# Kernel tuning notes

Measured on AMD Instinct MI355X. Metric: run time of the kernel, lower is better.

## Reference

```python
import jax, jax.numpy as jnp
import numpy as np

DELTA_VAR = 0.5
DELTA_DIST = 1.5
ALPHA, BETA, GAMMA = 1.0, 1.0, 0.001
EPS = 1e-8


def _safe_sqrt(x):
    # sqrt with zero (sub)gradient at 0, matching torch.norm's subgradient
    pos = x > 0
    return jnp.sqrt(jnp.where(pos, x, 1.0)) * pos


def setup_inputs() -> dict:
    key = jax.random.key(0)
    k1, k2, k3 = jax.random.split(key, 3)
    B, F, H, W, K = 8, 16, 384, 384, 24
    x = jax.random.normal(k1, (B, F, H, W), dtype=jnp.float32)
    n_clusters = jax.random.randint(k2, (B,), 2, K + 1).astype(jnp.int32)
    # per-pixel instance labels, in-range per sample
    labels = jax.random.randint(k3, (B, H * W), 0, K) % n_clusters[:, None]
    target = jax.nn.one_hot(labels, K, dtype=jnp.float32)  # (B, L, K)
    target = target.transpose(0, 2, 1).reshape(B, K, H, W)
    return {"input": x, "target": target, "n_clusters": n_clusters}


def reference(input, target, n_clusters):
    B, F, H, W = input.shape
    K = target.shape[1]
    x = input.reshape(B, F, H * W)          # (b, f, l)
    t = target.reshape(B, K, H * W)         # (b, c, l)
    nc = n_clusters.astype(x.dtype)         # (b,)
    valid = (jnp.arange(K)[None, :] < n_clusters[:, None]).astype(x.dtype)  # (b, c)

    # ---- cluster means (masked segment mean; padded clusters -> 0) ----
    t_sum = t.sum(-1)                                        # (b, c)
    sums = jnp.einsum('bfl,bcl->bfc', x, t)                  # (b, f, c)
    means = sums / (t_sum[:, None, :] + EPS) * valid[:, None, :]

    # ---- variance term: ||x_l - mu_c||_2 via quadratic expansion ----
    x2 = jnp.sum(x * x, axis=1)                              # (b, l)
    m2 = jnp.sum(means * means, axis=1)                      # (b, c)
    xm = jnp.einsum('bfl,bfc->bcl', x, means)                # (b, c, l)
    d2 = jnp.maximum(x2[:, None, :] - 2.0 * xm + m2[:, :, None], 0.0)
    dist = _safe_sqrt(d2)                                    # (b, c, l)
    var = jnp.maximum(dist - DELTA_VAR, 0.0) ** 2 * t        # (b, c, l)
    c_var = var.sum(-1) / (t_sum + EPS)                      # (b, c)
    var_per = (c_var * valid).sum(-1) / (nc + EPS)
    var_term = jnp.sum(var_per * (nc > 0)) / B

    # ---- distance term: hinge on pairwise mean distances ----
    mm = jnp.einsum('bfc,bfd->bcd', means, means)            # (b, c, c)
    pd2 = jnp.maximum(m2[:, :, None] - 2.0 * mm + m2[:, None, :], 0.0)
    pdist = _safe_sqrt(pd2)                                  # (b, c, c)
    offdiag = 1.0 - jnp.eye(K, dtype=x.dtype)
    pair_mask = valid[:, :, None] * valid[:, None, :] * offdiag
    hinge = jnp.maximum(2.0 * DELTA_DIST - pdist, 0.0) ** 2 * pair_mask
    dist_per = hinge.sum((1, 2)) / (2.0 * nc * (nc - 1.0) + EPS)
    dist_term = jnp.sum(dist_per * (nc > 1)) / B

    # ---- regularization term: mean over valid clusters of ||mu_c|| ----
    norms = _safe_sqrt(m2)                                   # (b, c)
    reg_term = jnp.sum((norms * valid).sum(-1) / nc) / B

    return ALPHA * var_term + BETA * dist_term + GAMMA * reg_term
```

## Files before the change

### kernel.cpp

```cpp
#include <hip/hip_runtime.h>

#define B 8
#define F 16
#define K 24
#define L 147456
#define CHUNK1 1024
#define NCH1 144
#define TOTCH 1152
#define EPSF 1e-8f
#define DELTA_VAR 0.5f
#define DELTA_DIST 1.5f
#define GAMMA 0.001f

typedef float fx4 __attribute__((ext_vector_type(4)));
typedef short bf16x8 __attribute__((ext_vector_type(8)));
typedef float f32x4 __attribute__((ext_vector_type(4)));

#define OFF_CNTP 1769472
#define OFF_VARP 1880064
#define OFF_CNT  1990656
#define OFF_MEAN 1991424
#define OFF_LAB  2003968

__device__ __forceinline__ short to_bf16(float v) {
    unsigned u = __float_as_uint(v);
    return (short)((u + 0x7FFFu + ((u >> 16) & 1u)) >> 16);
}

__global__ __launch_bounds__(256, 2) void k1_sums(
        const float* __restrict__ t, const float* __restrict__ x,
        unsigned char* __restrict__ labels, float* __restrict__ cnt_part,
        float* __restrict__ sum_part) {
    const int gblk = blockIdx.x;
    const int b = gblk / NCH1;
    const int ch = gblk % NCH1;
    const int tid = threadIdx.x;
    const int wave = tid >> 6;
    const int lane = tid & 63;

    __shared__ unsigned char slab[CHUNK1];
    __shared__ float hist[4][32];
    __shared__ float sacc[4][F * K];

    if (lane < 32) hist[wave][lane] = 0.f;

    const int px = ch * CHUNK1 + tid * 4;
    const fx4* t4 = (const fx4*)t;
    fx4 tv[K];
    #pragma unroll
    for (int c = 0; c < K; ++c)
        tv[c] = __builtin_nontemporal_load(&t4[((size_t)(b * K + c) * L + px) >> 2]);

    int lab0 = 0, lab1 = 0, lab2 = 0, lab3 = 0;
    #pragma unroll
    for (int c = 0; c < K; ++c) {
        lab0 += c * (tv[c].x > 0.5f);
        lab1 += c * (tv[c].y > 0.5f);
        lab2 += c * (tv[c].z > 0.5f);
        lab3 += c * (tv[c].w > 0.5f);
    }
    uchar4 lv = make_uchar4((unsigned char)lab0, (unsigned char)lab1,
                            (unsigned char)lab2, (unsigned char)lab3);
    *(uchar4*)&labels[(size_t)b * L + px] = lv;
    *(uchar4*)&slab[tid * 4] = lv;
    atomicAdd(&hist[wave][lab0], 1.f);
    atomicAdd(&hist[wave][lab1], 1.f);
    atomicAdd(&hist[wave][lab2], 1.f);
    atomicAdd(&hist[wave][lab3], 1.f);
    __syncthreads();
    if (tid < K) {
        float v = hist[0][tid] + hist[1][tid] + hist[2][tid] + hist[3][tid];
        cnt_part[tid * TOTCH + gblk] = v;
    }

    const int n = lane & 15;
    const int q = lane >> 4;
    const float* xr = x + (size_t)(b * F + n) * L + ch * CHUNK1 + wave * 256 + q * 8;
    fx4 xv[16];
    #pragma unroll
    for (int it = 0; it < 8; ++it) {
        xv[2 * it]     = *(const fx4*)(xr + it * 32);
        xv[2 * it + 1] = *(const fx4*)(xr + it * 32 + 4);
    }

    const unsigned char* sl = slab + wave * 256 + q * 8;
    f32x4 acc0 = {0.f, 0.f, 0.f, 0.f};
    f32x4 acc1 = {0.f, 0.f, 0.f, 0.f};
    #pragma unroll
    for (int it = 0; it < 8; ++it) {
        unsigned l0 = *(const unsigned*)(sl + it * 32);
        unsigned l1 = *(const unsigned*)(sl + it * 32 + 4);
        fx4 xa = xv[2 * it], xc = xv[2 * it + 1];

        bf16x8 afrag;
        afrag[0] = to_bf16(xa.x); afrag[1] = to_bf16(xa.y);
        afrag[2] = to_bf16(xa.z); afrag[3] = to_bf16(xa.w);
        afrag[4] = to_bf16(xc.x); afrag[5] = to_bf16(xc.y);
        afrag[6] = to_bf16(xc.z); afrag[7] = to_bf16(xc.w);

        bf16x8 bf0, bf1;
        #pragma unroll
        for (int j = 0; j < 8; ++j) {
            int lj = (j < 4) ? ((l0 >> (8 * j)) & 0xFF) : ((l1 >> (8 * (j - 4))) & 0xFF);
            bf0[j] = (lj == n)      ? (short)0x3F80 : (short)0;
            bf1[j] = (lj == n + 16) ? (short)0x3F80 : (short)0;
        }
        acc0 = __builtin_amdgcn_mfma_f32_16x16x32_bf16(afrag, bf0, acc0, 0, 0, 0);
        acc1 = __builtin_amdgcn_mfma_f32_16x16x32_bf16(afrag, bf1, acc1, 0, 0, 0);
    }

    #pragma unroll
    for (int r = 0; r < 4; ++r) {
        int f = q * 4 + r;
        sacc[wave][f * K + n] = acc0[r];
        if (n < 8) sacc[wave][f * K + 16 + n] = acc1[r];
    }
    __syncthreads();
    for (int i = tid; i < F * K; i += 256) {
        float v = sacc[0][i] + sacc[1][i] + sacc[2][i] + sacc[3][i];
        sum_part[(size_t)gblk * (F * K) + i] = v;
    }
}

__global__ __launch_bounds__(256) void k2_means(const float* __restrict__ cnt_part,
                                                const float* __restrict__ sum_part,
                                                const int* __restrict__ ncl,
                                                float* __restrict__ counts,
                                                float* __restrict__ means) {
    const int b = blockIdx.x;
    const int tid = threadIdx.x;
    __shared__ float cl[8][K];
    __shared__ float cs[K];

    if (tid < 192) {
        int c = tid >> 3, grp = tid & 7;
        const float* row = cnt_part + c * TOTCH + b * NCH1 + grp * 18;
        float s = 0.f;
        #pragma unroll
        for (int j = 0; j < 18; ++j) s += row[j];
        cl[grp][c] = s;
    }
    __syncthreads();
    if (tid < K) {
        float s = 0.f;
        #pragma unroll
        for (int g = 0; g < 8; ++g) s += cl[g][tid];
        cs[tid] = s;
        counts[b * K + tid] = s;
    }
    __syncthreads();
    const int ncb = ncl[b];
    for (int r = tid; r < F * K; r += 256) {
        float s = 0.f;
        const float* base = sum_part + (size_t)b * NCH1 * (F * K) + r;
        #pragma unroll 4
        for (int j = 0; j < NCH1; ++j) s += base[(size_t)j * (F * K)];
        int c = r % K;
        float valid = (c < ncb) ? 1.f : 0.f;
        means[b * F * K + r] = s / (cs[c] + EPSF) * valid;
    }
}

__global__ __launch_bounds__(256, 2) void k3_var(
        const float* __restrict__ x, const unsigned char* __restrict__ labels,
        const float* __restrict__ means, float* __restrict__ var_part) {
    const int gblk = blockIdx.x;
    const int b = gblk / NCH1;
    const int ch = gblk % NCH1;
    const int tid = threadIdx.x;
    const int wave = tid >> 6;
    const int lane = tid & 63;

    __shared__ float m[F * K];
    __shared__ float hist[4][32];

    const int px = ch * CHUNK1 + tid * 4;
    uchar4 lv = *(const uchar4*)&labels[(size_t)b * L + px];
    const fx4* x4 = (const fx4*)x;
    fx4 xv[F];
    #pragma unroll
    for (int f = 0; f < F; ++f)
        xv[f] = x4[((size_t)(b * F + f) * L + px) >> 2];

    for (int i = tid; i < F * K; i += 256) m[i] = means[b * F * K + i];
    if (lane < 32) hist[wave][lane] = 0.f;
    __syncthreads();

    float d0 = 0.f, d1 = 0.f, d2 = 0.f, d3 = 0.f;
    #pragma unroll
    for (int f = 0; f < F; ++f) {
        float u0 = xv[f].x - m[f * K + lv.x]; d0 += u0 * u0;
        float u1 = xv[f].y - m[f * K + lv.y]; d1 += u1 * u1;
        float u2 = xv[f].z - m[f * K + lv.z]; d2 += u2 * u2;
        float u3 = xv[f].w - m[f * K + lv.w]; d3 += u3 * u3;
    }
    float s0 = fmaxf(sqrtf(d0) - DELTA_VAR, 0.f); s0 *= s0;
    float s1 = fmaxf(sqrtf(d1) - DELTA_VAR, 0.f); s1 *= s1;
    float s2 = fmaxf(sqrtf(d2) - DELTA_VAR, 0.f); s2 *= s2;
    float s3 = fmaxf(sqrtf(d3) - DELTA_VAR, 0.f); s3 *= s3;
    atomicAdd(&hist[wave][lv.x], s0);
    atomicAdd(&hist[wave][lv.y], s1);
    atomicAdd(&hist[wave][lv.z], s2);
    atomicAdd(&hist[wave][lv.w], s3);
    __syncthreads();
    if (tid < K) {
        float v = hist[0][tid] + hist[1][tid] + hist[2][tid] + hist[3][tid];
        var_part[tid * TOTCH + gblk] = v;
    }
}

__global__ __launch_bounds__(256) void k4_finish(
        const float* __restrict__ var_part, const float* __restrict__ means,
        const float* __restrict__ counts, const int* __restrict__ ncl,
        float* __restrict__ out) {
    __shared__ float big[B * F * K];
    __shared__ float vs[192], cn[192], red[256];
    const int tid = threadIdx.x;

    for (int i = tid; i < B * F * K; i += 256) big[i] = means[i];
    if (tid < 192) {
        int bb = tid / K, c = tid % K;
        const float* row = var_part + c * TOTCH + bb * NCH1;
        float s = 0.f;
        #pragma unroll 4
        for (int j = 0; j < NCH1; ++j) s += row[j];
        vs[tid] = s;
        cn[tid] = counts[tid];
    }
    __syncthreads();

    float total = 0.f;
    for (int idx = tid; idx < B * K * K; idx += 256) {
        int bb = idx / (K * K);
        int r = idx % (K * K);
        int c = r / K;
        int d = r % K;
        int ncb = ncl[bb];
        float fnc = (float)ncb;
        if (d == 0 && c < ncb && ncb > 0) {
            float cv = vs[bb * K + c] / (cn[bb * K + c] + EPSF);
            total += cv / (fnc + EPSF) * (1.0f / B);
            float m2 = 0.f;
            #pragma unroll
            for (int f = 0; f < F; ++f) {
                float mv = big[(bb * F + f) * K + c];
                m2 += mv * mv;
            }
            total += GAMMA * sqrtf(m2) / fnc * (1.0f / B);
        }
        if (c != d && c < ncb && d < ncb && ncb > 1) {
            float pd2 = 0.f;
            #pragma unroll
            for (int f = 0; f < F; ++f) {
                float diff = big[(bb * F + f) * K + c] - big[(bb * F + f) * K + d];
                pd2 += diff * diff;
            }
            float h = fmaxf(2.f * DELTA_DIST - sqrtf(pd2), 0.f);
            total += h * h / (2.f * fnc * (fnc - 1.f) + EPSF) * (1.0f / B);
        }
    }
    red[tid] = total;
    __syncthreads();
    for (int s = 128; s > 0; s >>= 1) {
        if (tid < s) red[tid] += red[tid + s];
        __syncthreads();
    }
    if (tid == 0) out[0] = red[0];
}

extern "C" void kernel_launch(void* const* d_in, const int* in_sizes, int n_in,
                              void* d_out, int out_size, void* d_ws, size_t ws_size,
                              hipStream_t stream) {
    const float* x = (const float*)d_in[0];
    const float* t = (const float*)d_in[1];
    const int* ncl = (const int*)d_in[2];
    float* out = (float*)d_out;

    char* ws = (char*)d_ws;
    float* sum_part = (float*)ws;
    float* cnt_part = (float*)(ws + OFF_CNTP);
    float* var_part = (float*)(ws + OFF_VARP);
    float* counts   = (float*)(ws + OFF_CNT);
    float* means    = (float*)(ws + OFF_MEAN);
    unsigned char* labels = (unsigned char*)(ws + OFF_LAB);

    k1_sums <<<TOTCH, 256, 0, stream>>>(t, x, labels, cnt_part, sum_part);
    k2_means<<<B, 256, 0, stream>>>(cnt_part, sum_part, ncl, counts, means);
    k3_var  <<<TOTCH, 256, 0, stream>>>(x, labels, means, var_part);
    k4_finish<<<1, 256, 0, stream>>>(var_part, means, counts, ncl, out);
}
```

Before: 261.9 us.

## Parallelize means reduction, transpose partial sums, reorder loads and raise occupancy

k2_means previously ran on only 8 blocks with serial per-thread loops. It is now spread across 768 blocks, one wave per (batch, feature, cluster) entry reducing its 144 partials with shuffles; the sum_part layout is transposed so each wave reads contiguously. In k1 the x loads are issued before the target loads, the 24 target loads are split into three batches of 8 to reduce register pressure, and the occupancy hints on k1 and k3 are raised. sched_barriers pin load ordering, and one unroll factor is bumped. Higher occupancy hints risk register spills.

```diff
diff --git a/kernel.cpp b/kernel.cpp
--- a/kernel.cpp
+++ b/kernel.cpp
@@ -27,7 +27,7 @@
     return (short)((u + 0x7FFFu + ((u >> 16) & 1u)) >> 16);
 }
 
-__global__ __launch_bounds__(256, 2) void k1_sums(
+__global__ __launch_bounds__(256, 3) void k1_sums(
         const float* __restrict__ t, const float* __restrict__ x,
         unsigned char* __restrict__ labels, float* __restrict__ cnt_part,
         float* __restrict__ sum_part) {
@@ -37,6 +37,8 @@
     const int tid = threadIdx.x;
     const int wave = tid >> 6;
     const int lane = tid & 63;
+    const int n = lane & 15;
+    const int q = lane >> 4;
 
     __shared__ unsigned char slab[CHUNK1];
     __shared__ float hist[4][32];
@@ -44,20 +46,34 @@
 
     if (lane < 32) hist[wave][lane] = 0.f;
 
+    const float* xr = x + (size_t)(b * F + n) * L + ch * CHUNK1 + wave * 256 + q * 8;
+    fx4 xv[16];
+    #pragma unroll
+    for (int it = 0; it < 8; ++it) {
+        xv[2 * it]     = *(const fx4*)(xr + it * 32);
+        xv[2 * it + 1] = *(const fx4*)(xr + it * 32 + 4);
+    }
+    __builtin_amdgcn_sched_barrier(0);
+
     const int px = ch * CHUNK1 + tid * 4;
     const fx4* t4 = (const fx4*)t;
-    fx4 tv[K];
-    #pragma unroll
-    for (int c = 0; c < K; ++c)
-        tv[c] = __builtin_nontemporal_load(&t4[((size_t)(b * K + c) * L + px) >> 2]);
-
     int lab0 = 0, lab1 = 0, lab2 = 0, lab3 = 0;
     #pragma unroll
-    for (int c = 0; c < K; ++c) {
-        lab0 += c * (tv[c].x > 0.5f);
-        lab1 += c * (tv[c].y > 0.5f);
-        lab2 += c * (tv[c].z > 0.5f);
-        lab3 += c * (tv[c].w > 0.5f);
+    for (int h = 0; h < 3; ++h) {
+        fx4 tv[8];
+        #pragma unroll
+        for (int j = 0; j < 8; ++j)
+            tv[j] = __builtin_nontemporal_load(
+                &t4[((size_t)(b * K + h * 8 + j) * L + px) >> 2]);
+        __builtin_amdgcn_sched_barrier(0);
+        #pragma unroll
+        for (int j = 0; j < 8; ++j) {
+            int c = h * 8 + j;
+            lab0 += c * (tv[j].x > 0.5f);
+            lab1 += c * (tv[j].y > 0.5f);
+            lab2 += c * (tv[j].z > 0.5f);
+            lab3 += c * (tv[j].w > 0.5f);
+        }
     }
     uchar4 lv = make_uchar4((unsigned char)lab0, (unsigned char)lab1,
                             (unsigned char)lab2, (unsigned char)lab3);
@@ -73,16 +89,6 @@
         cnt_part[tid * TOTCH + gblk] = v;
     }
 
-    const int n = lane & 15;
-    const int q = lane >> 4;
-    const float* xr = x + (size_t)(b * F + n) * L + ch * CHUNK1 + wave * 256 + q * 8;
-    fx4 xv[16];
-    #pragma unroll
-    for (int it = 0; it < 8; ++it) {
-        xv[2 * it]     = *(const fx4*)(xr + it * 32);
-        xv[2 * it + 1] = *(const fx4*)(xr + it * 32 + 4);
-    }
-
     const unsigned char* sl = slab + wave * 256 + q * 8;
     f32x4 acc0 = {0.f, 0.f, 0.f, 0.f};
     f32x4 acc1 = {0.f, 0.f, 0.f, 0.f};
@@ -118,7 +124,7 @@
     __syncthreads();
     for (int i = tid; i < F * K; i += 256) {
         float v = sacc[0][i] + sacc[1][i] + sacc[2][i] + sacc[3][i];
-        sum_part[(size_t)gblk * (F * K) + i] = v;
+        sum_part[(size_t)i * TOTCH + gblk] = v;
     }
 }
 
@@ -127,41 +133,29 @@
                                                 const int* __restrict__ ncl,
                                                 float* __restrict__ counts,
                                                 float* __restrict__ means) {
-    const int b = blockIdx.x;
-    const int tid = threadIdx.x;
-    __shared__ float cl[8][K];
-    __shared__ float cs[K];
-
-    if (tid < 192) {
-        int c = tid >> 3, grp = tid & 7;
-        const float* row = cnt_part + c * TOTCH + b * NCH1 + grp * 18;
-        float s = 0.f;
-        #pragma unroll
-        for (int j = 0; j < 18; ++j) s += row[j];
-        cl[grp][c] = s;
-    }
-    __syncthreads();
-    if (tid < K) {
-        float s = 0.f;
-        #pragma unroll
-        for (int g = 0; g < 8; ++g) s += cl[g][tid];
-        cs[tid] = s;
-        counts[b * K + tid] = s;
-    }
-    __syncthreads();
-    const int ncb = ncl[b];
-    for (int r = tid; r < F * K; r += 256) {
-        float s = 0.f;
-        const float* base = sum_part + (size_t)b * NCH1 * (F * K) + r;
-        #pragma unroll 4
-        for (int j = 0; j < NCH1; ++j) s += base[(size_t)j * (F * K)];
-        int c = r % K;
-        float valid = (c < ncb) ? 1.f : 0.f;
-        means[b * F * K + r] = s / (cs[c] + EPSF) * valid;
-    }
-}
-
-__global__ __launch_bounds__(256, 2) void k3_var(
+    const int idx = blockIdx.x * 4 + (threadIdx.x >> 6);
+    const int lane = threadIdx.x & 63;
+    const int b = idx / (F * K);
+    const int r = idx % (F * K);
+    const int c = r % K;
+
+    const float* crow = cnt_part + c * TOTCH + b * NCH1;
+    const float* srow = sum_part + (size_t)r * TOTCH + b * NCH1;
+    float cv = crow[lane] + crow[lane + 64] + ((lane < 16) ? crow[lane + 128] : 0.f);
+    float sv = srow[lane] + srow[lane + 64] + ((lane < 16) ? srow[lane + 128] : 0.f);
+    #pragma unroll
+    for (int off = 32; off > 0; off >>= 1) {
+        cv += __shfl_down(cv, off);
+        sv += __shfl_down(sv, off);
+    }
+    if (lane == 0) {
+        if (r < K) counts[b * K + c] = cv;
+        float valid = (c < ncl[b]) ? 1.f : 0.f;
+        means[b * F * K + r] = sv / (cv + EPSF) * valid;
+    }
+}
+
+__global__ __launch_bounds__(256, 4) void k3_var(
         const float* __restrict__ x, const unsigned char* __restrict__ labels,
         const float* __restrict__ means, float* __restrict__ var_part) {
     const int gblk = blockIdx.x;
@@ -181,6 +175,7 @@
     #pragma unroll
     for (int f = 0; f < F; ++f)
         xv[f] = x4[((size_t)(b * F + f) * L + px) >> 2];
+    __builtin_amdgcn_sched_barrier(0);
 
     for (int i = tid; i < F * K; i += 256) m[i] = means[b * F * K + i];
     if (lane < 32) hist[wave][lane] = 0.f;
@@ -222,7 +217,7 @@
         int bb = tid / K, c = tid % K;
         const float* row = var_part + c * TOTCH + bb * NCH1;
         float s = 0.f;
-        #pragma unroll 4
+        #pragma unroll 8
         for (int j = 0; j < NCH1; ++j) s += row[j];
         vs[tid] = s;
         cn[tid] = counts[tid];
@@ -285,7 +280,7 @@
     unsigned char* labels = (unsigned char*)(ws + OFF_LAB);
 
     k1_sums <<<TOTCH, 256, 0, stream>>>(t, x, labels, cnt_part, sum_part);
-    k2_means<<<B, 256, 0, stream>>>(cnt_part, sum_part, ncl, counts, means);
+    k2_means<<<768, 256, 0, stream>>>(cnt_part, sum_part, ncl, counts, means);
     k3_var  <<<TOTCH, 256, 0, stream>>>(x, labels, means, var_part);
     k4_finish<<<1, 256, 0, stream>>>(var_part, means, counts, ncl, out);
 }
```

After: 243.6 us. 1.08x faster.
